# Kernel optimization log

Hardware: AMD Instinct MI355X
Metric: run time of the kernel (lower is better)

## Reference

```python
import jax, jax.numpy as jnp
import numpy as np

N_NODES = 50000
N_EDGES = 1600000
HIDDEN = 128
IN_DIM = 3  # x (1) + relative pos (2)


def setup_inputs() -> dict:
    key = jax.random.key(0)
    ks = jax.random.split(key, 5)
    x = jax.random.normal(ks[0], (N_NODES, 1), dtype=jnp.float32)
    pos = jax.random.normal(ks[1], (N_NODES, 2), dtype=jnp.float32)
    # MLP params (Linear(3,128) -> ReLU -> Linear(128,128)), fan-in scaled
    W1 = jax.random.normal(ks[2], (IN_DIM, HIDDEN), dtype=jnp.float32) / np.sqrt(IN_DIM)
    b1 = jnp.zeros((HIDDEN,), dtype=jnp.float32)
    W2 = jax.random.normal(ks[3], (HIDDEN, HIDDEN), dtype=jnp.float32) / np.sqrt(HIDDEN)
    b2 = jnp.zeros((HIDDEN,), dtype=jnp.float32)
    edge_index = jax.random.randint(ks[4], (2, N_EDGES), 0, N_NODES, dtype=jnp.int64)
    return {"x": x, "pos": pos, "W1": W1, "b1": b1, "W2": W2, "b2": b2,
            "edge_index": edge_index}


def reference(x, pos, W1, b1, W2, b2, edge_index):
    # PTConv with aggr='add': per-edge message = nn(cat([x_j, pos_j - pos_i]))
    # then scatter-add into destination node i.
    src = edge_index[0]  # j (neighbor / source)
    dst = edge_index[1]  # i (center / destination)
    msg_in = jnp.concatenate([x[src], pos[src] - pos[dst]], axis=-1)  # [E, 3]
    h = jax.nn.relu(msg_in @ W1 + b1) @ W2 + b2                        # [E, 128]
    out = jax.ops.segment_sum(h, dst, num_segments=x.shape[0])        # [N, 128]
    return out
```

## Files before the change

kernel.cpp:

```cpp
#include <hip/hip_runtime.h>


#define HIDDEN 128
#define BNODES 32
#define CAPB 2048
#define EPB 16384
#define SThr 512
#define CAP 1536
#define W2LD 136

typedef float v2f __attribute__((ext_vector_type(2)));
typedef short bf16x8 __attribute__((ext_vector_type(8)));
typedef float f32x4 __attribute__((ext_vector_type(4)));

__device__ __forceinline__ unsigned short f2bf(float f) {
    unsigned int u = __float_as_uint(f);
    u += 0x7fffu + ((u >> 16) & 1u);
    return (unsigned short)(u >> 16);
}

__global__ void k_init(int* __restrict__ bcur, int NB) {
    int i = blockIdx.x * blockDim.x + threadIdx.x;
    if (i < NB) bcur[i] = i * CAPB;
}

__global__ __launch_bounds__(SThr) void k_scatter(const int* __restrict__ src,
                                                  const int* __restrict__ dst,
                                                  int* __restrict__ bcur,
                                                  unsigned int* __restrict__ pairs,
                                                  int E, int NB) {
    extern __shared__ int hs[];
    int* h  = hs;
    int* hb = hs + NB;
    int tid = threadIdx.x;
    for (int i = tid; i < NB; i += SThr) h[i] = 0;
    __syncthreads();
    int base = blockIdx.x * EPB;
    int lim = base + EPB; if (lim > E) lim = E;
    for (int i = base + tid; i < lim; i += SThr) atomicAdd(&h[dst[i] >> 5], 1);
    __syncthreads();
    for (int i = tid; i < NB; i += SThr) {
        int c = h[i];
        hb[i] = c ? atomicAdd(&bcur[i], c) : 0;
        h[i] = 0;
    }
    __syncthreads();
    for (int i = base + tid; i < lim; i += SThr) {
        int d = dst[i];
        int bkt = d >> 5;
        int loc = atomicAdd(&h[bkt], 1);
        int slot = hb[bkt] + loc;
        if (slot < (bkt + 1) * CAPB)
            pairs[slot] = ((unsigned int)src[i] << 5) | (unsigned int)(d & 31);
    }
}

__global__ __launch_bounds__(256) void k_main(const float* __restrict__ x,
                                              const float* __restrict__ pos,
                                              const float* __restrict__ W1,
                                              const float* __restrict__ b1,
                                              const int* __restrict__ bcur,
                                              const unsigned int* __restrict__ pairs,
                                              float* __restrict__ agg,
                                              int* __restrict__ deg, int N) {
    __shared__ float4 f_s[CAP];
    __shared__ int cnt[BNODES];
    __shared__ int offn[BNODES + 1];
    __shared__ int cur[BNODES];

    int tid = threadIdx.x, lane = tid & 63, w = tid >> 6;
    int b = blockIdx.x;
    int n0 = b * BNODES;
    int e0 = b * CAPB;
    int ec = bcur[b] - e0; if (ec > CAPB) ec = CAPB;
    int e1 = e0 + ec;

    int c0 = 2 * lane;
    v2f w10 = { W1[c0],              W1[c0 + 1] };
    v2f w11 = { W1[HIDDEN + c0],     W1[HIDDEN + c0 + 1] };
    v2f w12 = { W1[2 * HIDDEN + c0], W1[2 * HIDDEN + c0 + 1] };
    v2f b1v = { b1[c0], b1[c0 + 1] };
    const v2f zero = { 0.f, 0.f };
    const float2* pos2 = (const float2*)pos;

    v2f acc[8];
    int dga[8];
    #pragma unroll
    for (int s = 0; s < 8; ++s) { acc[s] = zero; dga[s] = 0; }

    for (int cbeg = e0; cbeg < e1; cbeg += CAP) {
        int ccnt = e1 - cbeg; if (ccnt > CAP) ccnt = CAP;
        if (tid < BNODES) cnt[tid] = 0;
        __syncthreads();
        for (int i = tid; i < ccnt; i += 256) atomicAdd(&cnt[pairs[cbeg + i] & 31u], 1);
        __syncthreads();
        if (tid < BNODES) {
            int v = cnt[tid];
            int sc = v;
            #pragma unroll
            for (int d = 1; d < BNODES; d <<= 1) {
                int u = __shfl_up(sc, d);
                if (lane >= d) sc += u;
            }
            offn[tid + 1] = sc;
            if (tid == 0) offn[0] = 0;
            cur[tid] = sc - v;
        }
        __syncthreads();
        for (int i = tid; i < ccnt; i += 256) {
            unsigned int r = pairs[cbeg + i];
            int j = (int)(r >> 5);
            int local = (int)(r & 31u);
            float a = x[j];
            float2 pj = pos2[j];
            float2 pi = pos2[n0 + local];
            int p = atomicAdd(&cur[local], 1);
            f_s[p] = make_float4(a, pj.x - pi.x, pj.y - pi.y, 0.f);
        }
        __syncthreads();
        #pragma unroll
        for (int s = 0; s < 8; ++s) {
            int l = w * 8 + s;
            int sb = offn[l], se = offn[l + 1];
            if (sb < se) {
                dga[s] += se - sb;
                v2f A = acc[s];
                #pragma unroll 4
                for (int t = sb; t < se; ++t) {
                    float4 f = f_s[t];
                    v2f h = f.x * w10 + b1v;
                    h = f.y * w11 + h;
                    h = f.z * w12 + h;
                    h = __builtin_elementwise_max(h, zero);
                    A += h;
                }
                acc[s] = A;
            }
        }
        __syncthreads();
    }

    #pragma unroll
    for (int s = 0; s < 8; ++s) {
        int l = w * 8 + s;
        int node = n0 + l;
        if (node < N) {
            ((v2f*)&agg[(size_t)node * HIDDEN])[lane] = acc[s];
            if (lane == 0) deg[node] = dga[s];
        }
    }
}

__global__ __launch_bounds__(256) void k_w2(float* __restrict__ agg,
                                            const float* __restrict__ W2,
                                            const float* __restrict__ b2,
                                            const int* __restrict__ deg, int N) {
    __shared__ unsigned short w2t[HIDDEN * W2LD];
    int tid = threadIdx.x;
    for (int idx = tid; idx < HIDDEN * HIDDEN; idx += 256) {
        int k = idx >> 7, c = idx & 127;
        w2t[c * W2LD + k] = f2bf(W2[idx]);
    }
    __syncthreads();

    int lane = tid & 63, w = tid >> 6;
    int row0 = blockIdx.x * 64 + w * 16;
    if (row0 >= N) return;

    int rA = row0 + (lane & 15);
    int koff = (lane >> 4) * 8;
    bool okA = rA < N;

    bf16x8 a[4];
    #pragma unroll
    for (int k0 = 0; k0 < 4; ++k0) {
        float4 fa = {0.f,0.f,0.f,0.f}, fb = {0.f,0.f,0.f,0.f};
        if (okA) {
            const float4* p = (const float4*)&agg[(size_t)rA * HIDDEN + k0 * 32 + koff];
            fa = p[0]; fb = p[1];
        }
        bf16x8 v;
        v[0] = (short)f2bf(fa.x); v[1] = (short)f2bf(fa.y);
        v[2] = (short)f2bf(fa.z); v[3] = (short)f2bf(fa.w);
        v[4] = (short)f2bf(fb.x); v[5] = (short)f2bf(fb.y);
        v[6] = (short)f2bf(fb.z); v[7] = (short)f2bf(fb.w);
        a[k0] = v;
    }

    f32x4 acc[8];
    #pragma unroll
    for (int ct = 0; ct < 8; ++ct) acc[ct] = (f32x4){0.f,0.f,0.f,0.f};

    #pragma unroll
    for (int ct = 0; ct < 8; ++ct) {
        int col = ct * 16 + (lane & 15);
        #pragma unroll
        for (int k0 = 0; k0 < 4; ++k0) {
            bf16x8 bfrag = *(const bf16x8*)&w2t[col * W2LD + k0 * 32 + koff];
            acc[ct] = __builtin_amdgcn_mfma_f32_16x16x32_bf16(a[k0], bfrag, acc[ct], 0, 0, 0);
        }
    }

    int mbase = row0 + (lane >> 4) * 4;
    float dg[4];
    #pragma unroll
    for (int i = 0; i < 4; ++i) dg[i] = (mbase + i < N) ? (float)deg[mbase + i] : 0.f;

    #pragma unroll
    for (int ct = 0; ct < 8; ++ct) {
        int col = ct * 16 + (lane & 15);
        float b2c = b2[col];
        #pragma unroll
        for (int i = 0; i < 4; ++i) {
            int r = mbase + i;
            if (r < N) agg[(size_t)r * HIDDEN + col] = acc[ct][i] + dg[i] * b2c;
        }
    }
}

extern "C" void kernel_launch(void* const* d_in, const int* in_sizes, int n_in,
                              void* d_out, int out_size, void* d_ws, size_t ws_size,
                              hipStream_t stream) {
    const float* x   = (const float*)d_in[0];
    const float* pos = (const float*)d_in[1];
    const float* W1  = (const float*)d_in[2];
    const float* b1  = (const float*)d_in[3];
    const float* W2  = (const float*)d_in[4];
    const float* b2  = (const float*)d_in[5];
    const int*   ei  = (const int*)d_in[6];

    int N = in_sizes[0];
    int E = in_sizes[6] / 2;
    const int* src = ei;
    const int* dst = ei + E;
    float* out = (float*)d_out;

    int NB = (N + BNODES - 1) / BNODES;

    int* bcur = (int*)d_ws;
    int* deg  = bcur + NB;
    unsigned int* pairs = (unsigned int*)(deg + N);

    int gribs = (E + EPB - 1) / EPB;
    size_t scatLds = 2u * (size_t)NB * sizeof(int);

    k_init<<<(NB + 255) / 256, 256, 0, stream>>>(bcur, NB);
    k_scatter<<<gribs, SThr, scatLds, stream>>>(src, dst, bcur, pairs, E, NB);
    k_main<<<NB, 256, 0, stream>>>(x, pos, W1, b1, bcur, pairs, out, deg, N);
    k_w2<<<(N + 63) / 64, 256, 0, stream>>>(out, W2, b2, deg, N);
}
```

Baseline: 107.7 us.

## Replace single-pass edge bucketing with two-level radix scatter via super-buckets

The one-pass scatter into 1563 fine buckets, which needed a large LDS histogram per block and scattered writes across many buckets, is replaced by two passes. The first pass scatters edges into 49 super-buckets of 1024 nodes, and the second splits each super-bucket into 32-node buckets for the main kernel. The aim is better write locality and a cheaper histogram in the scatter. In exchange it adds a kernel launch, an extra read and write of all edge pairs, and a smaller per-bucket capacity (1536) that may drop edges when a bucket overflows.

```diff
diff --git a/kernel.cpp b/kernel.cpp
--- a/kernel.cpp
+++ b/kernel.cpp
@@ -3,9 +3,11 @@
 
 #define HIDDEN 128
 #define BNODES 32
-#define CAPB 2048
-#define EPB 16384
-#define SThr 512
+#define SUPSH 10
+#define CAPA 36864
+#define CAPF 1536
+#define EPBA 2048
+#define KSUB 16
 #define CAP 1536
 #define W2LD 136
 
@@ -19,39 +21,76 @@
     return (unsigned short)(u >> 16);
 }
 
-__global__ void k_init(int* __restrict__ bcur, int NB) {
+__global__ void k_init(int* __restrict__ bcurA, int* __restrict__ bcurF,
+                       int NSUP, int NB) {
     int i = blockIdx.x * blockDim.x + threadIdx.x;
-    if (i < NB) bcur[i] = i * CAPB;
-}
-
-__global__ __launch_bounds__(SThr) void k_scatter(const int* __restrict__ src,
-                                                  const int* __restrict__ dst,
-                                                  int* __restrict__ bcur,
-                                                  unsigned int* __restrict__ pairs,
-                                                  int E, int NB) {
-    extern __shared__ int hs[];
-    int* h  = hs;
-    int* hb = hs + NB;
+    if (i < NSUP) bcurA[i] = i * CAPA;
+    if (i < NB)   bcurF[i] = i * CAPF;
+}
+
+__global__ __launch_bounds__(256) void k_scatA(const int* __restrict__ src,
+                                               const int* __restrict__ dst,
+                                               int* __restrict__ bcurA,
+                                               unsigned int* __restrict__ pairsA,
+                                               int E, int NSUP) {
+    __shared__ int h[64];
+    __shared__ int hb[64];
     int tid = threadIdx.x;
-    for (int i = tid; i < NB; i += SThr) h[i] = 0;
-    __syncthreads();
-    int base = blockIdx.x * EPB;
-    int lim = base + EPB; if (lim > E) lim = E;
-    for (int i = base + tid; i < lim; i += SThr) atomicAdd(&h[dst[i] >> 5], 1);
-    __syncthreads();
-    for (int i = tid; i < NB; i += SThr) {
-        int c = h[i];
-        hb[i] = c ? atomicAdd(&bcur[i], c) : 0;
-        h[i] = 0;
-    }
-    __syncthreads();
-    for (int i = base + tid; i < lim; i += SThr) {
+    if (tid < 64) h[tid] = 0;
+    __syncthreads();
+    int base = blockIdx.x * EPBA;
+    int lim = base + EPBA; if (lim > E) lim = E;
+    for (int i = base + tid; i < lim; i += 256) atomicAdd(&h[dst[i] >> SUPSH], 1);
+    __syncthreads();
+    if (tid < NSUP) {
+        int c = h[tid];
+        hb[tid] = c ? atomicAdd(&bcurA[tid], c) : 0;
+        h[tid] = 0;
+    }
+    __syncthreads();
+    for (int i = base + tid; i < lim; i += 256) {
         int d = dst[i];
-        int bkt = d >> 5;
-        int loc = atomicAdd(&h[bkt], 1);
-        int slot = hb[bkt] + loc;
-        if (slot < (bkt + 1) * CAPB)
-            pairs[slot] = ((unsigned int)src[i] << 5) | (unsigned int)(d & 31);
+        int s = d >> SUPSH;
+        int loc = atomicAdd(&h[s], 1);
+        int slot = hb[s] + loc;
+        if (slot < (s + 1) * CAPA)
+            pairsA[slot] = ((unsigned int)src[i] << SUPSH) | (unsigned int)(d & 1023);
+    }
+}
+
+__global__ __launch_bounds__(256) void k_scatB(const int* __restrict__ bcurA,
+                                               const unsigned int* __restrict__ pairsA,
+                                               int* __restrict__ bcurF,
+                                               unsigned int* __restrict__ pairsF,
+                                               int NB) {
+    __shared__ int h[32];
+    __shared__ int hb[32];
+    int tid = threadIdx.x;
+    int s = blockIdx.x / KSUB;
+    int k = blockIdx.x % KSUB;
+    int base0 = s * CAPA;
+    int ec = bcurA[s] - base0; if (ec > CAPA) ec = CAPA;
+    int slice = (ec + KSUB - 1) / KSUB;
+    int lo = base0 + k * slice;
+    int hi = lo + slice; { int e1 = base0 + ec; if (hi > e1) hi = e1; }
+    if (tid < 32) h[tid] = 0;
+    __syncthreads();
+    for (int i = lo + tid; i < hi; i += 256) atomicAdd(&h[(pairsA[i] >> 5) & 31u], 1);
+    __syncthreads();
+    if (tid < 32) {
+        int c = h[tid];
+        hb[tid] = c ? atomicAdd(&bcurF[s * 32 + tid], c) : 0;
+        h[tid] = 0;
+    }
+    __syncthreads();
+    for (int i = lo + tid; i < hi; i += 256) {
+        unsigned int e = pairsA[i];
+        int fbl = (int)((e >> 5) & 31u);
+        int fb = s * 32 + fbl;
+        int loc = atomicAdd(&h[fbl], 1);
+        int slot = hb[fbl] + loc;
+        if (slot < (fb + 1) * CAPF)
+            pairsF[slot] = ((e >> SUPSH) << 5) | (e & 31u);
     }
 }
 
@@ -59,7 +98,7 @@
                                               const float* __restrict__ pos,
                                               const float* __restrict__ W1,
                                               const float* __restrict__ b1,
-                                              const int* __restrict__ bcur,
+                                              const int* __restrict__ bcurF,
                                               const unsigned int* __restrict__ pairs,
                                               float* __restrict__ agg,
                                               int* __restrict__ deg, int N) {
@@ -71,8 +110,8 @@
     int tid = threadIdx.x, lane = tid & 63, w = tid >> 6;
     int b = blockIdx.x;
     int n0 = b * BNODES;
-    int e0 = b * CAPB;
-    int ec = bcur[b] - e0; if (ec > CAPB) ec = CAPB;
+    int e0 = b * CAPF;
+    int ec = bcurF[b] - e0; if (ec > CAPF) ec = CAPF;
     int e1 = e0 + ec;
 
     int c0 = 2 * lane;
@@ -235,17 +274,20 @@
     const int* dst = ei + E;
     float* out = (float*)d_out;
 
-    int NB = (N + BNODES - 1) / BNODES;
-
-    int* bcur = (int*)d_ws;
-    int* deg  = bcur + NB;
-    unsigned int* pairs = (unsigned int*)(deg + N);
-
-    int gribs = (E + EPB - 1) / EPB;
-    size_t scatLds = 2u * (size_t)NB * sizeof(int);
-
-    k_init<<<(NB + 255) / 256, 256, 0, stream>>>(bcur, NB);
-    k_scatter<<<gribs, SThr, scatLds, stream>>>(src, dst, bcur, pairs, E, NB);
-    k_main<<<NB, 256, 0, stream>>>(x, pos, W1, b1, bcur, pairs, out, deg, N);
+    int NB   = (N + BNODES - 1) / BNODES;
+    int NSUP = (N + 1023) >> SUPSH;
+
+    int* bcurA = (int*)d_ws;
+    int* bcurF = bcurA + 64;
+    int* deg   = bcurF + NB;
+    unsigned int* pairsA = (unsigned int*)(deg + N);
+    unsigned int* pairsF = pairsA + (size_t)NSUP * CAPA;
+
+    int gribsA = (E + EPBA - 1) / EPBA;
+
+    k_init<<<(NB + 255) / 256, 256, 0, stream>>>(bcurA, bcurF, NSUP, NB);
+    k_scatA<<<gribsA, 256, 0, stream>>>(src, dst, bcurA, pairsA, E, NSUP);
+    k_scatB<<<NSUP * KSUB, 256, 0, stream>>>(bcurA, pairsA, bcurF, pairsF, NB);
+    k_main<<<NB, 256, 0, stream>>>(x, pos, W1, b1, bcurF, pairsF, out, deg, N);
     k_w2<<<(N + 63) / 64, 256, 0, stream>>>(out, W2, b2, deg, N);
 }
```

After: 106.5 us. About the same (-1.1%).
